# Kernel optimization log

Measured on AMD Instinct MI355X. Metric: run time of the kernel, lower is better.

Reference implementation:

```python
import jax, jax.numpy as jnp
import numpy as np

B, D, H, S = 4096, 512, 512, 16
EVENT_THRESH = 0.85  # hard-coded in original forward (e_t > 0.85), tau unused


def setup_inputs() -> dict:
    key = jax.random.key(0)
    ks = jax.random.split(key, 17)
    s = 0.02
    return {
        "x_t": jax.random.normal(ks[0], (B, D), jnp.float32),
        "h_lstm": jax.random.normal(ks[1], (B, H), jnp.float32),
        "c_lstm": jax.random.normal(ks[2], (B, H), jnp.float32),
        "slots": jax.random.normal(ks[3], (B, S, D), jnp.float32),
        "ptr": jax.random.randint(ks[4], (B,), 0, S, jnp.int32),
        # SequenceMemoryCell params
        "value_W": jax.random.normal(ks[5], (D, D), jnp.float32) * s,
        "value_b": jnp.zeros((D,), jnp.float32),
        "ed_W": jax.random.normal(ks[6], (1, D), jnp.float32) * s,
        "ed_b": jnp.zeros((1,), jnp.float32),
        "pos_emb": jax.random.normal(ks[7], (S, D), jnp.float32),
        "lstm_Wih": jax.random.normal(ks[8], (4 * H, D), jnp.float32) * s,
        "lstm_Whh": jax.random.normal(ks[9], (4 * H, H), jnp.float32) * s,
        "lstm_bih": jnp.zeros((4 * H,), jnp.float32),
        "lstm_bhh": jnp.zeros((4 * H,), jnp.float32),
        # outer hand-written LSTM params
        "Wih": jax.random.normal(ks[10], (4 * H, D + H), jnp.float32) * s,
        "bih": jnp.zeros((4 * H,), jnp.float32),
        "Whh": jax.random.normal(ks[11], (4 * H, H), jnp.float32) * s,
    }


def reference(x_t, h_lstm, c_lstm, slots, value_W, value_b, ed_W, ed_b,
              pos_emb, lstm_Wih, lstm_Whh, lstm_bih, lstm_bhh,
              Wih, bih, Whh, ptr):
    b, n_slots, d = slots.shape
    h = lstm_Whh.shape[1]
    # --- SequenceMemoryCell ---
    e_t = jax.nn.sigmoid(x_t @ ed_W.T + ed_b)            # (B, 1)
    event = e_t > EVENT_THRESH                            # (B, 1) bool
    v = x_t @ value_W.T + value_b                         # (B, D)
    # conditional pointer-indexed write into circular slot buffer
    write = (jnp.arange(n_slots)[None, :] == ptr[:, None]) & event  # (B, S)
    new_slots = jnp.where(write[:, :, None], v[:, None, :], slots)
    new_ptr = (ptr + event[:, 0].astype(ptr.dtype)) % n_slots
    slots_pe = new_slots + pos_emb[None, :, :]            # (B, S, D)
    # slot-fuser LSTM over n_slots (PyTorch gate order i,f,g,o), h0=c0=0
    def step(carry, x_s):
        hh, cc = carry
        g = x_s @ lstm_Wih.T + lstm_bih + hh @ lstm_Whh.T + lstm_bhh
        i, f, gg, o = jnp.split(g, 4, axis=1)
        cc = jax.nn.sigmoid(f) * cc + jax.nn.sigmoid(i) * jnp.tanh(gg)
        hh = jax.nn.sigmoid(o) * jnp.tanh(cc)
        return (hh, cc), None
    h0 = jnp.zeros((b, h), slots.dtype)
    (h_mem, _), _ = jax.lax.scan(step, (h0, h0), jnp.swapaxes(slots_pe, 0, 1))
    # --- outer hand-written LSTM cell on [x_t; h_mem] ---
    gates = jnp.concatenate([x_t, h_mem], axis=1) @ Wih.T + bih + h_lstm @ Whh.T
    i, f, g_t, o = jnp.split(gates, 4, axis=1)
    c_new = jax.nn.sigmoid(f) * c_lstm + jax.nn.sigmoid(i) * jnp.tanh(g_t)
    h_new = jax.nn.sigmoid(o) * jnp.tanh(c_new)
    return (h_new, c_new, h_mem, new_slots, new_ptr)
```

## Files before the change

kernel.cpp:

```cpp
#include <hip/hip_runtime.h>
#include <hip/hip_bf16.h>

constexpr int kB = 4096;
constexpr int kD = 512;
constexpr int kH = 512;
constexpr int kS = 16;
constexpr int kG = 2048;
constexpr int kChainBlocks = 256;

typedef __attribute__((ext_vector_type(8))) short bf16x8_t;
typedef __attribute__((ext_vector_type(4))) float f32x4_t;

__device__ __forceinline__ short f2bf(float x) {
  __hip_bfloat16 h = __float2bfloat16(x);
  return *reinterpret_cast<short*>(&h);
}
__device__ __forceinline__ float sigm(float x) { return 1.0f / (1.0f + expf(-x)); }

__device__ __forceinline__ int swz(int row, int kElem) {
  return row * 64 + (((kElem >> 3) ^ (row & 7)) << 3);
}
__device__ __forceinline__ int wswz(int wrow, int kElem) {
  return wrow * 1024 + ((((kElem >> 3) ^ wrow) & 7) << 3) + (kElem & ~63) ;
}

__global__ void bar_init_kernel(unsigned* __restrict__ ctr, int n)
{
  int i = blockIdx.x * blockDim.x + threadIdx.x;
  if (i < n) ctr[i] = 0u;
}

__global__ void event_kernel(const float* __restrict__ x,
                             const float* __restrict__ edW,
                             const float* __restrict__ edb,
                             const int* __restrict__ ptr,
                             int* __restrict__ ev,
                             float* __restrict__ newptr_out)
{
  int b = blockIdx.x * 4 + (threadIdx.x >> 6);
  int lane = threadIdx.x & 63;
  const float* xr = x + (size_t)b * kD;
  float sum = 0.f;
  for (int k = lane; k < kD; k += 64) sum += xr[k] * edW[k];
  #pragma unroll
  for (int off = 32; off; off >>= 1) sum += __shfl_down(sum, off, 64);
  if (lane == 0) {
    float e = sigm(sum + edb[0]);
    int evt = (e > 0.85f) ? 1 : 0;
    ev[b] = evt;
    newptr_out[b] = (float)((ptr[b] + evt) & (kS - 1));
  }
}

__global__ void f2b_kernel(const float* __restrict__ src, short* __restrict__ dst, int n4)
{
  int i = blockIdx.x * blockDim.x + threadIdx.x;
  if (i >= n4) return;
  const float4 v = reinterpret_cast<const float4*>(src)[i];
  short4 o;
  o.x = f2bf(v.x); o.y = f2bf(v.y); o.z = f2bf(v.z); o.w = f2bf(v.w);
  reinterpret_cast<short4*>(dst)[i] = o;
}

__global__ void packw_gates_kernel(const float* __restrict__ W1, int w1,
                                   const float* __restrict__ W2, int w2,
                                   short* __restrict__ dst, int total4)
{
  int i = blockIdx.x * blockDim.x + threadIdx.x;
  if (i >= total4) return;
  long e = (long)i * 4;
  int K = w1 + w2;
  long p = e / K;
  int col = (int)(e - p * K);
  long r = (long)(((p >> 4) & 3) * 512 + ((p >> 6) << 4) + (p & 15));
  const float* src = (col < w1) ? (W1 + r * (long)w1 + col)
                                : (W2 + r * (long)w2 + (col - w1));
  const float4 v = *reinterpret_cast<const float4*>(src);
  short4 o; o.x=f2bf(v.x); o.y=f2bf(v.y); o.z=f2bf(v.z); o.w=f2bf(v.w);
  *reinterpret_cast<short4*>(dst + e) = o;
}

__global__ void packbias_kernel(const float* __restrict__ b1, const float* __restrict__ b2,
                                float* __restrict__ o, int n)
{
  int p = blockIdx.x * blockDim.x + threadIdx.x;
  if (p >= n) return;
  int r = ((p >> 4) & 3) * 512 + ((p >> 6) << 4) + (p & 15);
  float v = b1[r];
  if (b2) v += b2[r];
  o[p] = v;
}

__global__ void slot_update_kernel(const float* __restrict__ slots,
                                   const float* __restrict__ v,
                                   const float* __restrict__ pos_emb,
                                   const int* __restrict__ ptr,
                                   const int* __restrict__ ev,
                                   float* __restrict__ new_slots,
                                   short* __restrict__ slots_pe)
{
  size_t i = (size_t)blockIdx.x * blockDim.x + threadIdx.x;
  size_t e = i * 4;
  int d = (int)(e & (kD - 1));
  size_t bs = e >> 9;
  int s = (int)(bs & (kS - 1));
  size_t b = bs >> 4;
  float4 val;
  if (ev[b] && (ptr[b] == s)) val = *reinterpret_cast<const float4*>(v + (b << 9) + d);
  else                        val = *reinterpret_cast<const float4*>(slots + e);
  *reinterpret_cast<float4*>(new_slots + e) = val;
  const float4 pe = *reinterpret_cast<const float4*>(pos_emb + ((size_t)s << 9) + d);
  short4 o;
  o.x = f2bf(val.x + pe.x); o.y = f2bf(val.y + pe.y);
  o.z = f2bf(val.z + pe.z); o.w = f2bf(val.w + pe.w);
  *reinterpret_cast<short4*>(slots_pe + e) = o;
}

__global__ __launch_bounds__(512, 2)
void chain_kernel(const short* __restrict__ slots_pe,
                  const short* __restrict__ W,
                  const float* __restrict__ bias,
                  short* __restrict__ hsteps,
                  float* __restrict__ hmem,
                  unsigned* __restrict__ barrier_ctr)
{
  __shared__ short Wlds[64 * 1024];
  const int tid  = threadIdx.x;
  const int wave = tid >> 6;
  const int lane = tid & 63;

  const int bx  = blockIdx.x & 7;
  const int by  = blockIdx.x >> 3;
  const int row0 = bx * 512;
  const int col0 = by * 64;

  #pragma unroll
  for (int r8 = 0; r8 < 8; ++r8) {
    const int wrow = r8 * 8 + wave;
    #pragma unroll
    for (int p = 0; p < 2; ++p) {
      const int c = p * 64 + lane;
      const short* src = W + (size_t)(col0 + wrow) * 1024 + ((c ^ (wrow & 7)) << 3);
      __builtin_amdgcn_global_load_lds(
          (const __attribute__((address_space(1))) void*)src,
          (__attribute__((address_space(3))) void*)&Wlds[wrow * 1024 + p * 512],
          16, 0, 0);
    }
  }
  __syncthreads();

  float bv[4];
  #pragma unroll
  for (int n = 0; n < 4; ++n)
    bv[n] = bias[col0 + n * 16 + (lane & 15)];
  const int hcol = by * 16 + (lane & 15);
  const int rowsbase = row0 + wave * 64;
  const int arow = rowsbase + (lane & 15);
  const int klane = (lane >> 4) << 3;

  float c_reg[4][4];
  #pragma unroll
  for (int m = 0; m < 4; ++m)
    #pragma unroll
    for (int r = 0; r < 4; ++r) c_reg[m][r] = 0.f;

  for (int s = 0; s < kS; ++s) {
    f32x4_t acc[4][4];
    #pragma unroll
    for (int m = 0; m < 4; ++m)
      #pragma unroll
      for (int n = 0; n < 4; ++n) acc[m][n] = {0.f, 0.f, 0.f, 0.f};

    {
      const short* Ap = slots_pe + (size_t)s * kD + (size_t)arow * (kS * kD);
      #pragma unroll 4
      for (int k0 = 0; k0 < 512; k0 += 32) {
        const int kc = k0 + klane;
        bf16x8_t af[4], bfr[4];
        #pragma unroll
        for (int m = 0; m < 4; ++m)
          af[m] = *reinterpret_cast<const bf16x8_t*>(Ap + (size_t)(m * 16) * (kS * kD) + kc);
        #pragma unroll
        for (int n = 0; n < 4; ++n)
          bfr[n] = *reinterpret_cast<const bf16x8_t*>(&Wlds[wswz((lane & 15) + n * 16, kc)]);
        #pragma unroll
        for (int m = 0; m < 4; ++m)
          #pragma unroll
          for (int n = 0; n < 4; ++n)
            acc[m][n] = __builtin_amdgcn_mfma_f32_16x16x32_bf16(af[m], bfr[n], acc[m][n], 0, 0, 0);
      }
    }

    if (s > 0) {
      unsigned* ctr = barrier_ctr + (((s - 1) * 8 + bx) << 4);
      __syncthreads();
      if (tid == 0) {
        __hip_atomic_fetch_add(ctr, 1u, __ATOMIC_RELEASE, __HIP_MEMORY_SCOPE_AGENT);
        while (__hip_atomic_load(ctr, __ATOMIC_RELAXED, __HIP_MEMORY_SCOPE_AGENT) < 32u)
          __builtin_amdgcn_s_sleep(2);
      }
      __syncthreads();
      const short* Hp = hsteps + (size_t)(s - 1) * kB * kH + (size_t)arow * kH;
      #pragma unroll 4
      for (int k0 = 0; k0 < 512; k0 += 32) {
        const int kc = k0 + klane;
        bf16x8_t af[4], bfr[4];
        #pragma unroll
        for (int m = 0; m < 4; ++m)
          af[m] = *reinterpret_cast<const bf16x8_t*>(Hp + (size_t)(m * 16) * kH + kc);
        #pragma unroll
        for (int n = 0; n < 4; ++n)
          bfr[n] = *reinterpret_cast<const bf16x8_t*>(&Wlds[wswz((lane & 15) + n * 16, 512 + kc)]);
        #pragma unroll
        for (int m = 0; m < 4; ++m)
          #pragma unroll
          for (int n = 0; n < 4; ++n)
            acc[m][n] = __builtin_amdgcn_mfma_f32_16x16x32_bf16(af[m], bfr[n], acc[m][n], 0, 0, 0);
      }
    }

    short* Hout = hsteps + (size_t)s * kB * kH;
    #pragma unroll
    for (int m = 0; m < 4; ++m) {
      const int rbase = rowsbase + m * 16 + (lane >> 4) * 4;
      #pragma unroll
      for (int r = 0; r < 4; ++r) {
        const size_t idx = (size_t)(rbase + r) * kH + hcol;
        const float gi = acc[m][0][r] + bv[0];
        const float gf = acc[m][1][r] + bv[1];
        const float gg = acc[m][2][r] + bv[2];
        const float go = acc[m][3][r] + bv[3];
        const float cn = sigm(gf) * c_reg[m][r] + sigm(gi) * tanhf(gg);
        const float hn = sigm(go) * tanhf(cn);
        c_reg[m][r] = cn;
        Hout[idx] = f2bf(hn);
        if (s == kS - 1) hmem[idx] = hn;
      }
    }
  }
}

__global__ __launch_bounds__(256, 4)
void gemm_fused_kernel(const short* __restrict__ A0, int lda0,
                       const short* __restrict__ A1, int lda1,
                       const short* __restrict__ A2, int lda2,
                       int nseg, const short* __restrict__ W, int ldw,
                       const float* __restrict__ bias, int mode, int nby,
                       float* __restrict__ C, int ldc,
                       const float* __restrict__ c_in,
                       float* __restrict__ h_out, float* __restrict__ c_out)
{
  __shared__ short As[128 * 64];
  __shared__ short Ws[64 * 64];
  const int tid  = threadIdx.x;
  const int wave = tid >> 6;
  const int lane = tid & 63;

  const int nb  = gridDim.x;
  const int vid = (blockIdx.x & 7) * (nb >> 3) + (blockIdx.x >> 3);
  const int bx  = vid / nby;
  const int by  = vid - bx * nby;
  const int row0 = bx * 128;
  const int col0 = by * 64;
  const int K = nseg << 9;

  f32x4_t acc[2][4];
  #pragma unroll
  for (int m = 0; m < 2; ++m)
    #pragma unroll
    for (int n = 0; n < 4; ++n)
      acc[m][n] = {0.f, 0.f, 0.f, 0.f};

  const int srow   = tid >> 3;
  const int scol   = (tid & 7) * 8;
  const int schunk = (((tid >> 3) ^ tid) & 7) * 8;

  for (int k0 = 0; k0 < K; k0 += 64) {
    const int seg = k0 >> 9;
    const int ks  = k0 & 511;
    const short* Ap = (seg == 0) ? A0 : ((seg == 1) ? A1 : A2);
    const int   lda = (seg == 0) ? lda0 : ((seg == 1) ? lda1 : lda2);
    __syncthreads();
    #pragma unroll
    for (int j = 0; j < 4; ++j) {
      const int r = j * 32 + srow;
      const short* asrc = Ap + (size_t)(row0 + r) * lda + ks + schunk;
      __builtin_amdgcn_global_load_lds(
          (const __attribute__((address_space(1))) void*)asrc,
          (__attribute__((address_space(3))) void*)&As[r * 64 + scol], 16, 0, 0);
    }
    #pragma unroll
    for (int j = 0; j < 2; ++j) {
      const int r = j * 32 + srow;
      const short* wsrc = W + (size_t)(col0 + r) * ldw + k0 + schunk;
      __builtin_amdgcn_global_load_lds(
          (const __attribute__((address_space(1))) void*)wsrc,
          (__attribute__((address_space(3))) void*)&Ws[r * 64 + scol], 16, 0, 0);
    }
    __syncthreads();
    #pragma unroll
    for (int kk = 0; kk < 64; kk += 32) {
      bf16x8_t af[2], bfr[4];
      const int kcol = kk + (lane >> 4) * 8;
      const int ar = wave * 32 + (lane & 15);
      const int br = lane & 15;
      #pragma unroll
      for (int m = 0; m < 2; ++m)
        af[m] = *reinterpret_cast<const bf16x8_t*>(&As[swz(ar + m * 16, kcol)]);
      #pragma unroll
      for (int n = 0; n < 4; ++n)
        bfr[n] = *reinterpret_cast<const bf16x8_t*>(&Ws[swz(br + n * 16, kcol)]);
      #pragma unroll
      for (int m = 0; m < 2; ++m)
        #pragma unroll
        for (int n = 0; n < 4; ++n)
          acc[m][n] = __builtin_amdgcn_mfma_f32_16x16x32_bf16(af[m], bfr[n], acc[m][n], 0, 0, 0);
    }
  }

  float bv[4];
  #pragma unroll
  for (int n = 0; n < 4; ++n)
    bv[n] = bias[col0 + n * 16 + (lane & 15)];

  if (mode == 0) {
    #pragma unroll
    for (int n = 0; n < 4; ++n) {
      const int col = col0 + n * 16 + (lane & 15);
      #pragma unroll
      for (int m = 0; m < 2; ++m) {
        const int rbase = row0 + wave * 32 + m * 16 + (lane >> 4) * 4;
        #pragma unroll
        for (int r = 0; r < 4; ++r)
          C[(size_t)(rbase + r) * ldc + col] = acc[m][n][r] + bv[n];
      }
    }
    return;
  }

  const int hcol = (col0 >> 6) * 16 + (lane & 15);
  #pragma unroll
  for (int m = 0; m < 2; ++m) {
    const int rbase = row0 + wave * 32 + m * 16 + (lane >> 4) * 4;
    #pragma unroll
    for (int r = 0; r < 4; ++r) {
      const size_t idx = (size_t)(rbase + r) * kH + hcol;
      const float gi = acc[m][0][r] + bv[0];
      const float gf = acc[m][1][r] + bv[1];
      const float gg = acc[m][2][r] + bv[2];
      const float go = acc[m][3][r] + bv[3];
      const float cn = sigm(gf) * c_in[idx] + sigm(gi) * tanhf(gg);
      const float hn = sigm(go) * tanhf(cn);
      c_out[idx] = cn;
      h_out[idx] = hn;
    }
  }
}

extern "C" void kernel_launch(void* const* d_in, const int* in_sizes, int n_in,
                              void* d_out, int out_size, void* d_ws, size_t ws_size,
                              hipStream_t stream)
{
  const float* x_t      = (const float*)d_in[0];
  const float* h_lstm   = (const float*)d_in[1];
  const float* c_lstm   = (const float*)d_in[2];
  const float* slots    = (const float*)d_in[3];
  const int*   ptr      = (const int*)  d_in[4];
  const float* value_W  = (const float*)d_in[5];
  const float* value_b  = (const float*)d_in[6];
  const float* ed_W     = (const float*)d_in[7];
  const float* ed_b     = (const float*)d_in[8];
  const float* pos_emb  = (const float*)d_in[9];
  const float* lstm_Wih = (const float*)d_in[10];
  const float* lstm_Whh = (const float*)d_in[11];
  const float* lstm_bih = (const float*)d_in[12];
  const float* lstm_bhh = (const float*)d_in[13];
  const float* Wih      = (const float*)d_in[14];
  const float* bih      = (const float*)d_in[15];
  const float* Whh      = (const float*)d_in[16];

  float* out       = (float*)d_out;
  float* h_new     = out;
  float* c_new     = out + (size_t)kB * kH;
  float* h_mem     = out + (size_t)2 * kB * kH;
  float* new_slots = out + (size_t)3 * kB * kH;
  float* new_ptr   = out + (size_t)3 * kB * kH + (size_t)kB * kS * kD;

  char* ws = (char*)d_ws;
  size_t off = 0;
  auto alloc = [&](size_t bytes) { void* p = ws + off; off += (bytes + 255) & ~(size_t)255; return p; };
  int*      ev        = (int*)     alloc((size_t)kB * 4);
  unsigned* bar       = (unsigned*)alloc((size_t)15 * 8 * 16 * 4);
  short*    x_b       = (short*)   alloc((size_t)kB * kD * 2);
  short*    hlstm_b   = (short*)   alloc((size_t)kB * kH * 2);
  short*    vW_b      = (short*)   alloc((size_t)kD * kD * 2);
  short*    stepW_b   = (short*)   alloc((size_t)kG * (kD + kH) * 2);
  float*    stepBias  = (float*)   alloc((size_t)kG * 4);
  short*    outerW_b  = (short*)   alloc((size_t)kG * (kD + kH + kH) * 2);
  float*    outerBias = (float*)   alloc((size_t)kG * 4);
  float*    v_f32     = (float*)   alloc((size_t)kB * kD * 4);
  short*    hsteps    = (short*)   alloc((size_t)kS * kB * kH * 2);
  short*    slots_pe  = (short*)   alloc((size_t)kB * kS * kD * 2);
  (void)ws_size; (void)in_sizes; (void)n_in; (void)out_size;

  bar_init_kernel<<<(15 * 8 * 16 + 255) / 256, 256, 0, stream>>>(bar, 15 * 8 * 16);

  event_kernel<<<kB / 4, 256, 0, stream>>>(x_t, ed_W, ed_b, ptr, ev, new_ptr);

  f2b_kernel<<<(kB * kD / 4 + 255) / 256, 256, 0, stream>>>(x_t, x_b, kB * kD / 4);
  f2b_kernel<<<(kB * kH / 4 + 255) / 256, 256, 0, stream>>>(h_lstm, hlstm_b, kB * kH / 4);
  f2b_kernel<<<(kD * kD / 4 + 255) / 256, 256, 0, stream>>>(value_W, vW_b, kD * kD / 4);
  packw_gates_kernel<<<(kG * 1024 / 4 + 255) / 256, 256, 0, stream>>>(
      lstm_Wih, kD, lstm_Whh, kH, stepW_b, kG * 1024 / 4);
  packw_gates_kernel<<<(kG * 1536 / 4 + 255) / 256, 256, 0, stream>>>(
      Wih, kD + kH, Whh, kH, outerW_b, kG * 1536 / 4);
  packbias_kernel<<<(kG + 255) / 256, 256, 0, stream>>>(lstm_bih, lstm_bhh, stepBias, kG);
  packbias_kernel<<<(kG + 255) / 256, 256, 0, stream>>>(bih, nullptr, outerBias, kG);

  gemm_fused_kernel<<<(kB / 128) * (kD / 64), 256, 0, stream>>>(
      x_b, kD, nullptr, 0, nullptr, 0, 1, vW_b, kD, value_b, 0, kD / 64,
      v_f32, kD, nullptr, nullptr, nullptr);

  slot_update_kernel<<<(int)((size_t)kB * kS * kD / 4 / 256), 256, 0, stream>>>(
      slots, v_f32, pos_emb, ptr, ev, new_slots, slots_pe);

  chain_kernel<<<kChainBlocks, 512, 0, stream>>>(
      slots_pe, stepW_b, stepBias, hsteps, h_mem, bar);

  gemm_fused_kernel<<<(kB / 128) * (kG / 64), 256, 0, stream>>>(
      x_b, kD, hsteps + (size_t)(kS - 1) * kB * kH, kH, hlstm_b, kH, 3,
      outerW_b, kD + kH + kH, outerBias, 2, kG / 64,
      nullptr, 0, c_lstm, h_new, c_new);
}
```

Before: 803.7 us.

## Signal chain barrier right after writing h, prefetch A fragments, use fast exp/tanh

Moves the per-step barrier arrival in the slot-fuser LSTM chain kernel to just after each block writes its hidden state, instead of after the next step's input GEMM. Peer blocks can then proceed as soon as data is ready, and the wait no longer sits behind redundant work. It also double-buffers global A-fragment loads two k-steps ahead in both GEMM loops. Sigmoid and tanh switch to __expf-based approximations in the gate epilogues, while the event threshold keeps the precise sigmoid, trading a little accuracy for cheaper transcendentals.

```diff
diff --git a/kernel.cpp b/kernel.cpp
--- a/kernel.cpp
+++ b/kernel.cpp
@@ -15,13 +15,19 @@
   __hip_bfloat16 h = __float2bfloat16(x);
   return *reinterpret_cast<short*>(&h);
 }
-__device__ __forceinline__ float sigm(float x) { return 1.0f / (1.0f + expf(-x)); }
+__device__ __forceinline__ float sigm_precise(float x) { return 1.0f / (1.0f + expf(-x)); }
+__device__ __forceinline__ float sigm(float x) { return 1.0f / (1.0f + __expf(-x)); }
+__device__ __forceinline__ float ftanh(float x) {
+  x = fminf(15.0f, fmaxf(-15.0f, x));
+  const float e = __expf(2.0f * x);
+  return (e - 1.0f) / (e + 1.0f);
+}
 
 __device__ __forceinline__ int swz(int row, int kElem) {
   return row * 64 + (((kElem >> 3) ^ (row & 7)) << 3);
 }
 __device__ __forceinline__ int wswz(int wrow, int kElem) {
-  return wrow * 1024 + ((((kElem >> 3) ^ wrow) & 7) << 3) + (kElem & ~63) ;
+  return wrow * 1024 + ((((kElem >> 3) ^ wrow) & 7) << 3) + (kElem & ~63);
 }
 
 __global__ void bar_init_kernel(unsigned* __restrict__ ctr, int n)
@@ -45,7 +51,7 @@
   #pragma unroll
   for (int off = 32; off; off >>= 1) sum += __shfl_down(sum, off, 64);
   if (lane == 0) {
-    float e = sigm(sum + edb[0]);
+    float e = sigm_precise(sum + edb[0]);
     int evt = (e > 0.85f) ? 1 : 0;
     ev[b] = evt;
     newptr_out[b] = (float)((ptr[b] + evt) & (kS - 1));
@@ -173,13 +179,23 @@
 
     {
       const short* Ap = slots_pe + (size_t)s * kD + (size_t)arow * (kS * kD);
+      bf16x8_t a0[4], a1[4];
+      #pragma unroll
+      for (int m = 0; m < 4; ++m) {
+        a0[m] = *reinterpret_cast<const bf16x8_t*>(Ap + (size_t)(m * 16) * (kS * kD) + klane);
+        a1[m] = *reinterpret_cast<const bf16x8_t*>(Ap + (size_t)(m * 16) * (kS * kD) + 32 + klane);
+      }
       #pragma unroll 4
       for (int k0 = 0; k0 < 512; k0 += 32) {
+        bf16x8_t an[4];
+        if (k0 + 64 < 512) {
+          #pragma unroll
+          for (int m = 0; m < 4; ++m)
+            an[m] = *reinterpret_cast<const bf16x8_t*>(
+                Ap + (size_t)(m * 16) * (kS * kD) + k0 + 64 + klane);
+        }
         const int kc = k0 + klane;
-        bf16x8_t af[4], bfr[4];
-        #pragma unroll
-        for (int m = 0; m < 4; ++m)
-          af[m] = *reinterpret_cast<const bf16x8_t*>(Ap + (size_t)(m * 16) * (kS * kD) + kc);
+        bf16x8_t bfr[4];
         #pragma unroll
         for (int n = 0; n < 4; ++n)
           bfr[n] = *reinterpret_cast<const bf16x8_t*>(&Wlds[wswz((lane & 15) + n * 16, kc)]);
@@ -187,27 +203,37 @@
         for (int m = 0; m < 4; ++m)
           #pragma unroll
           for (int n = 0; n < 4; ++n)
-            acc[m][n] = __builtin_amdgcn_mfma_f32_16x16x32_bf16(af[m], bfr[n], acc[m][n], 0, 0, 0);
+            acc[m][n] = __builtin_amdgcn_mfma_f32_16x16x32_bf16(a0[m], bfr[n], acc[m][n], 0, 0, 0);
+        #pragma unroll
+        for (int m = 0; m < 4; ++m) { a0[m] = a1[m]; a1[m] = an[m]; }
       }
     }
 
     if (s > 0) {
       unsigned* ctr = barrier_ctr + (((s - 1) * 8 + bx) << 4);
-      __syncthreads();
       if (tid == 0) {
-        __hip_atomic_fetch_add(ctr, 1u, __ATOMIC_RELEASE, __HIP_MEMORY_SCOPE_AGENT);
         while (__hip_atomic_load(ctr, __ATOMIC_RELAXED, __HIP_MEMORY_SCOPE_AGENT) < 32u)
           __builtin_amdgcn_s_sleep(2);
       }
       __syncthreads();
       const short* Hp = hsteps + (size_t)(s - 1) * kB * kH + (size_t)arow * kH;
+      bf16x8_t a0[4], a1[4];
+      #pragma unroll
+      for (int m = 0; m < 4; ++m) {
+        a0[m] = *reinterpret_cast<const bf16x8_t*>(Hp + (size_t)(m * 16) * kH + klane);
+        a1[m] = *reinterpret_cast<const bf16x8_t*>(Hp + (size_t)(m * 16) * kH + 32 + klane);
+      }
       #pragma unroll 4
       for (int k0 = 0; k0 < 512; k0 += 32) {
+        bf16x8_t an[4];
+        if (k0 + 64 < 512) {
+          #pragma unroll
+          for (int m = 0; m < 4; ++m)
+            an[m] = *reinterpret_cast<const bf16x8_t*>(
+                Hp + (size_t)(m * 16) * kH + k0 + 64 + klane);
+        }
         const int kc = k0 + klane;
-        bf16x8_t af[4], bfr[4];
-        #pragma unroll
-        for (int m = 0; m < 4; ++m)
-          af[m] = *reinterpret_cast<const bf16x8_t*>(Hp + (size_t)(m * 16) * kH + kc);
+        bf16x8_t bfr[4];
         #pragma unroll
         for (int n = 0; n < 4; ++n)
           bfr[n] = *reinterpret_cast<const bf16x8_t*>(&Wlds[wswz((lane & 15) + n * 16, 512 + kc)]);
@@ -215,7 +241,9 @@
         for (int m = 0; m < 4; ++m)
           #pragma unroll
           for (int n = 0; n < 4; ++n)
-            acc[m][n] = __builtin_amdgcn_mfma_f32_16x16x32_bf16(af[m], bfr[n], acc[m][n], 0, 0, 0);
+            acc[m][n] = __builtin_amdgcn_mfma_f32_16x16x32_bf16(a0[m], bfr[n], acc[m][n], 0, 0, 0);
+        #pragma unroll
+        for (int m = 0; m < 4; ++m) { a0[m] = a1[m]; a1[m] = an[m]; }
       }
     }
 
@@ -230,12 +258,19 @@
         const float gf = acc[m][1][r] + bv[1];
         const float gg = acc[m][2][r] + bv[2];
         const float go = acc[m][3][r] + bv[3];
-        const float cn = sigm(gf) * c_reg[m][r] + sigm(gi) * tanhf(gg);
-        const float hn = sigm(go) * tanhf(cn);
+        const float cn = sigm(gf) * c_reg[m][r] + sigm(gi) * ftanh(gg);
+        const float hn = sigm(go) * ftanh(cn);
         c_reg[m][r] = cn;
         Hout[idx] = f2bf(hn);
         if (s == kS - 1) hmem[idx] = hn;
       }
+    }
+
+    if (s < kS - 1) {
+      __syncthreads();
+      if (tid == 0)
+        __hip_atomic_fetch_add(barrier_ctr + ((s * 8 + bx) << 4), 1u,
+                               __ATOMIC_RELEASE, __HIP_MEMORY_SCOPE_AGENT);
     }
   }
 }
@@ -349,8 +384,8 @@
       const float gf = acc[m][1][r] + bv[1];
       const float gg = acc[m][2][r] + bv[2];
       const float go = acc[m][3][r] + bv[3];
-      const float cn = sigm(gf) * c_in[idx] + sigm(gi) * tanhf(gg);
-      const float hn = sigm(go) * tanhf(cn);
+      const float cn = sigm(gf) * c_in[idx] + sigm(gi) * ftanh(gg);
+      const float hn = sigm(go) * ftanh(cn);
       c_out[idx] = cn;
       h_out[idx] = hn;
     }
```

Result: faster. 753.3 us (-6.3%).
